# Kernel tuning notes

Measured on AMD Instinct MI355X. Metric: run time of the kernel, lower is better.

## Reference

```python
import jax, jax.numpy as jnp
import numpy as np

B, N, HC, HH, K, D = 64, 300, 64, 64, 3, 10

def setup_inputs() -> dict:
    key = jax.random.key(0)
    ks = jax.random.split(key, 8)
    inp = {
        "z": jax.random.normal(ks[0], (B, N, HC), dtype=jnp.float32),
        "W_in": jax.random.normal(ks[1], (HH, HC), dtype=jnp.float32) / np.sqrt(HC),
        "b_in": jax.random.normal(ks[2], (HH,), dtype=jnp.float32) * 0.01,
        "W_out": jax.random.normal(ks[3], (HC * HC, HH), dtype=jnp.float32) / np.sqrt(HH),
        "b_out": jax.random.normal(ks[4], (HC * HC,), dtype=jnp.float32) * 0.01,
        "node_emb": jax.random.normal(ks[5], (N, D), dtype=jnp.float32),
        "weights_pool": jax.random.normal(ks[6], (D, K, HH, HH), dtype=jnp.float32) / np.sqrt(D * HH),
        "bias_pool": jax.random.normal(ks[7], (D, HH), dtype=jnp.float32) * 0.01,
    }
    return inp

def _agc(z, node_emb, weights_pool, bias_pool):
    n = node_emb.shape[0]
    # data-adaptive adjacency: softmax over rows of relu(E E^T)
    supports = jax.nn.softmax(jax.nn.relu(node_emb @ node_emb.T), axis=1)  # [N,N]
    support_set = [jnp.eye(n, dtype=z.dtype), supports]
    for _ in range(2, K):  # Chebyshev recursion T_k = 2A T_{k-1} - T_{k-2}
        support_set.append(2.0 * supports @ support_set[-1] - support_set[-2])
    S = jnp.stack(support_set, axis=0)  # [K,N,N]
    weights = jnp.einsum('nd,dkio->nkio', node_emb, weights_pool)  # [N,K,HH,HH]
    bias = node_emb @ bias_pool  # [N,HH]
    x_g = jnp.einsum('knm,bmc->bnkc', S, z)  # [B,N,K,HH]
    return jnp.einsum('bnki,nkio->bno', x_g, weights) + bias

def reference(z, W_in, b_in, W_out, b_out, node_emb, weights_pool, bias_pool):
    h = jax.nn.relu(z @ W_in.T + b_in)                  # [B,N,HH]
    h = _agc(h, node_emb, weights_pool, bias_pool)      # [B,N,HH]
    out = (h @ W_out.T + b_out).reshape(B, N, HC, HC)   # [B,N,HC,HC]
    return jnp.tanh(out)
```

## Files before the change

kernel.cpp:

```cpp
#include <hip/hip_runtime.h>
#include <hip/hip_bf16.h>

#define BB 64
#define NN 300
#define HH 64
#define RTOT (BB*NN)
#define KIO  (3*HH*HH)
#define JOUT (HH*HH)

typedef __attribute__((ext_vector_type(8))) _Float16 f16x8;
typedef __attribute__((ext_vector_type(4))) float floatx4;

__device__ inline float tanh_fast(float x) {
    float e = __expf(2.f * x);
    return 1.f - 2.f * __builtin_amdgcn_rcpf(e + 1.f);
}

__global__ __launch_bounds__(256) void k_pre(const float* __restrict__ E,
                                             const float* __restrict__ z,
                                             const float* __restrict__ Win,
                                             const float* __restrict__ bin,
                                             const float* __restrict__ Wout,
                                             const float* __restrict__ pool,
                                             const float* __restrict__ bpool,
                                             float* __restrict__ A,
                                             float* __restrict__ h,
                                             float* __restrict__ Wn,
                                             float* __restrict__ bN,
                                             _Float16* __restrict__ Wh) {
    __shared__ float smem[8576];
    int bid = blockIdx.x, tid = threadIdx.x;

    if (bid < 300) {
        float* sE  = smem;
        float* row = smem + 16;
        float* red = smem + 320;
        int n = bid;
        if (tid < 10) sE[tid] = E[n*10 + tid];
        __syncthreads();
        float lmax = -1e30f;
        for (int m = tid; m < NN; m += 256) {
            float s = 0.f;
            #pragma unroll
            for (int d = 0; d < 10; ++d) s += sE[d] * E[m*10 + d];
            s = fmaxf(s, 0.f);
            row[m] = s;
            lmax = fmaxf(lmax, s);
        }
        red[tid] = lmax; __syncthreads();
        for (int off = 128; off > 0; off >>= 1) {
            if (tid < off) red[tid] = fmaxf(red[tid], red[tid+off]);
            __syncthreads();
        }
        float mx = red[0]; __syncthreads();
        float lsum = 0.f;
        for (int m = tid; m < NN; m += 256) {
            float e = __expf(row[m] - mx);
            row[m] = e;
            lsum += e;
        }
        red[tid] = lsum; __syncthreads();
        for (int off = 128; off > 0; off >>= 1) {
            if (tid < off) red[tid] += red[tid+off];
            __syncthreads();
        }
        float inv = 1.f / red[0];
        for (int m = tid; m < NN; m += 256) A[n*NN + m] = row[m] * inv;
    } else if (bid < 600) {
        float* Wt = smem;
        float* zl = smem + 4352;
        int tx = tid & 15, ty = tid >> 4;
        int r0 = (bid - 300) * 64;
        for (int e = tid; e < 4096; e += 256) {
            int o = e >> 6, c = e & 63;
            Wt[c*68 + o] = Win[e];
            zl[o*66 + c] = z[(size_t)(r0 + o)*64 + c];
        }
        __syncthreads();
        float4 bo = *(const float4*)&bin[tx*4];
        float acc[4][4];
        #pragma unroll
        for (int s = 0; s < 4; ++s) { acc[s][0]=bo.x; acc[s][1]=bo.y; acc[s][2]=bo.z; acc[s][3]=bo.w; }
        const float* zr = &zl[(ty*4)*66];
        for (int c = 0; c < 64; ++c) {
            float4 w = *(const float4*)&Wt[c*68 + tx*4];
            float z0 = zr[c], z1 = zr[66+c], z2 = zr[132+c], z3 = zr[198+c];
            acc[0][0] += z0*w.x; acc[0][1] += z0*w.y; acc[0][2] += z0*w.z; acc[0][3] += z0*w.w;
            acc[1][0] += z1*w.x; acc[1][1] += z1*w.y; acc[1][2] += z1*w.z; acc[1][3] += z1*w.w;
            acc[2][0] += z2*w.x; acc[2][1] += z2*w.y; acc[2][2] += z2*w.z; acc[2][3] += z2*w.w;
            acc[3][0] += z3*w.x; acc[3][1] += z3*w.y; acc[3][2] += z3*w.z; acc[3][3] += z3*w.w;
        }
        #pragma unroll
        for (int s = 0; s < 4; ++s) {
            float4 v = make_float4(fmaxf(acc[s][0],0.f), fmaxf(acc[s][1],0.f),
                                   fmaxf(acc[s][2],0.f), fmaxf(acc[s][3],0.f));
            *(float4*)&h[(size_t)(r0 + ty*4 + s)*64 + tx*4] = v;
        }
    } else if (bid < 675) {
        int idx = (bid - 600)*256 + tid;
        int n = idx >> 6, o = idx & 63;
        float s = 0.f;
        #pragma unroll
        for (int d = 0; d < 10; ++d) s += E[n*10 + d] * bpool[d*64 + o];
        bN[idx] = s;
    } else if (bid < 1699) {
        int idx = (bid - 675)*256 + tid;
        Wh[idx] = (_Float16)Wout[idx];
    } else {
        int idx = (bid - 1699)*256 + tid;
        int n = idx / KIO, kio = idx % KIO;
        float s = 0.f;
        #pragma unroll
        for (int d = 0; d < 10; ++d) s += E[n*10 + d] * pool[d*KIO + kio];
        Wn[idx] = s;
    }
}

__global__ __launch_bounds__(256) void k_spatialA(const float* __restrict__ A,
                                                  const float* __restrict__ h,
                                                  float* __restrict__ xg1) {
    int tid = threadIdx.x;
    int c = tid & 63;
    int w = __builtin_amdgcn_readfirstlane(tid >> 6);
    int b = blockIdx.y;
    int r0 = blockIdx.x * 20 + w * 5;
    const float* S = A + (size_t)r0 * NN;
    const float* hb = h + (size_t)b * NN * 64 + c;
    float a0 = 0.f, a1 = 0.f, a2 = 0.f, a3 = 0.f, a4 = 0.f;
    for (int m = 0; m < NN; m += 4) {
        float4 s0 = *(const float4*)(S + 0*NN + m);
        float4 s1 = *(const float4*)(S + 1*NN + m);
        float4 s2 = *(const float4*)(S + 2*NN + m);
        float4 s3 = *(const float4*)(S + 3*NN + m);
        float4 s4 = *(const float4*)(S + 4*NN + m);
        float h0 = hb[(m+0)*64];
        float h1 = hb[(m+1)*64];
        float h2 = hb[(m+2)*64];
        float h3 = hb[(m+3)*64];
        a0 = fmaf(s0.x,h0,a0); a0 = fmaf(s0.y,h1,a0); a0 = fmaf(s0.z,h2,a0); a0 = fmaf(s0.w,h3,a0);
        a1 = fmaf(s1.x,h0,a1); a1 = fmaf(s1.y,h1,a1); a1 = fmaf(s1.z,h2,a1); a1 = fmaf(s1.w,h3,a1);
        a2 = fmaf(s2.x,h0,a2); a2 = fmaf(s2.y,h1,a2); a2 = fmaf(s2.z,h2,a2); a2 = fmaf(s2.w,h3,a2);
        a3 = fmaf(s3.x,h0,a3); a3 = fmaf(s3.y,h1,a3); a3 = fmaf(s3.z,h2,a3); a3 = fmaf(s3.w,h3,a3);
        a4 = fmaf(s4.x,h0,a4); a4 = fmaf(s4.y,h1,a4); a4 = fmaf(s4.z,h2,a4); a4 = fmaf(s4.w,h3,a4);
    }
    float* dst = xg1 + ((size_t)b * NN + r0) * 64 + c;
    dst[0*64] = a0; dst[1*64] = a1; dst[2*64] = a2; dst[3*64] = a3; dst[4*64] = a4;
}

__global__ __launch_bounds__(256) void k_spatialB(const float* __restrict__ A,
                                                  const float* __restrict__ xg1,
                                                  const float* __restrict__ h,
                                                  float* __restrict__ xg2) {
    int tid = threadIdx.x;
    int c = tid & 63;
    int w = __builtin_amdgcn_readfirstlane(tid >> 6);
    int b = blockIdx.y;
    int r0 = blockIdx.x * 20 + w * 5;
    const float* S = A + (size_t)r0 * NN;
    const float* xb = xg1 + (size_t)b * NN * 64 + c;
    float a0 = 0.f, a1 = 0.f, a2 = 0.f, a3 = 0.f, a4 = 0.f;
    for (int m = 0; m < NN; m += 4) {
        float4 s0 = *(const float4*)(S + 0*NN + m);
        float4 s1 = *(const float4*)(S + 1*NN + m);
        float4 s2 = *(const float4*)(S + 2*NN + m);
        float4 s3 = *(const float4*)(S + 3*NN + m);
        float4 s4 = *(const float4*)(S + 4*NN + m);
        float x0 = xb[(m+0)*64];
        float x1 = xb[(m+1)*64];
        float x2 = xb[(m+2)*64];
        float x3 = xb[(m+3)*64];
        a0 = fmaf(s0.x,x0,a0); a0 = fmaf(s0.y,x1,a0); a0 = fmaf(s0.z,x2,a0); a0 = fmaf(s0.w,x3,a0);
        a1 = fmaf(s1.x,x0,a1); a1 = fmaf(s1.y,x1,a1); a1 = fmaf(s1.z,x2,a1); a1 = fmaf(s1.w,x3,a1);
        a2 = fmaf(s2.x,x0,a2); a2 = fmaf(s2.y,x1,a2); a2 = fmaf(s2.z,x2,a2); a2 = fmaf(s2.w,x3,a2);
        a3 = fmaf(s3.x,x0,a3); a3 = fmaf(s3.y,x1,a3); a3 = fmaf(s3.z,x2,a3); a3 = fmaf(s3.w,x3,a3);
        a4 = fmaf(s4.x,x0,a4); a4 = fmaf(s4.y,x1,a4); a4 = fmaf(s4.z,x2,a4); a4 = fmaf(s4.w,x3,a4);
    }
    const float* hb = h   + ((size_t)b * NN + r0) * 64 + c;
    float*       dst = xg2 + ((size_t)b * NN + r0) * 64 + c;
    dst[0*64] = 2.f*a0 - hb[0*64];
    dst[1*64] = 2.f*a1 - hb[1*64];
    dst[2*64] = 2.f*a2 - hb[2*64];
    dst[3*64] = 2.f*a3 - hb[3*64];
    dst[4*64] = 2.f*a4 - hb[4*64];
}

__global__ __launch_bounds__(256) void k_node_mm(const float* __restrict__ h,
                                                 const float* __restrict__ xg1,
                                                 const float* __restrict__ xg2,
                                                 const float* __restrict__ Wn,
                                                 const float* __restrict__ bN,
                                                 _Float16* __restrict__ h2h) {
    __shared__ float Wnl[192*64];
    __shared__ float xgl[8][192];
    int tid = threadIdx.x;
    int o = tid & 63, ty = tid >> 6;
    int n = blockIdx.x, b0 = blockIdx.y*8;
    for (int e = tid; e < 12288; e += 256) Wnl[e] = Wn[(size_t)n*KIO + e];
    for (int e = tid; e < 8*192; e += 256) {
        int bb = e / 192, ki = e % 192;
        int k = ki >> 6, i = ki & 63;
        const float* src = (k == 0) ? h : ((k == 1) ? xg1 : xg2);
        xgl[bb][ki] = src[((b0+bb)*NN + n)*64 + i];
    }
    __syncthreads();
    float bias = bN[n*64 + o];
    for (int bb = ty; bb < 8; bb += 4) {
        float acc = bias;
        for (int ki = 0; ki < 192; ++ki) acc += xgl[bb][ki] * Wnl[ki*64 + o];
        h2h[((b0+bb)*NN + n)*64 + o] = (_Float16)acc;
    }
}

__global__ __launch_bounds__(256) void k_out_proj_mfma(const _Float16* __restrict__ h2h,
                                                       const _Float16* __restrict__ Wh,
                                                       const float* __restrict__ bout,
                                                       float* __restrict__ out) {
    int tid  = threadIdx.x;
    int wave = tid >> 6, lane = tid & 63;
    int quad = lane >> 4, lr = lane & 15;
    int m0 = blockIdx.y*128 + (wave >> 1)*64;
    int n0 = blockIdx.x*128 + (wave & 1)*64;
    floatx4 acc[4][4] = {};
    const _Float16* Aptr = h2h + (size_t)(m0 + lr)*64 + quad*8;
    const _Float16* Bptr = Wh  + (size_t)(n0 + lr)*64 + quad*8;
    #pragma unroll
    for (int ks = 0; ks < 2; ++ks) {
        f16x8 a[4], b[4];
        #pragma unroll
        for (int f = 0; f < 4; ++f) {
            a[f] = *(const f16x8*)(Aptr + (size_t)f*16*64 + ks*32);
            b[f] = *(const f16x8*)(Bptr + (size_t)f*16*64 + ks*32);
        }
        #pragma unroll
        for (int mf = 0; mf < 4; ++mf)
            #pragma unroll
            for (int nf = 0; nf < 4; ++nf)
                acc[mf][nf] = __builtin_amdgcn_mfma_f32_16x16x32_f16(a[mf], b[nf], acc[mf][nf], 0, 0, 0);
    }
    #pragma unroll
    for (int nf = 0; nf < 4; ++nf) {
        int col = n0 + nf*16 + lr;
        float bj = bout[col];
        #pragma unroll
        for (int mf = 0; mf < 4; ++mf) {
            int row = m0 + mf*16 + quad*4;
            #pragma unroll
            for (int r = 0; r < 4; ++r) {
                float v = tanh_fast(acc[mf][nf][r] + bj);
                __builtin_nontemporal_store(v, &out[(size_t)(row + r)*JOUT + col]);
            }
        }
    }
}

extern "C" void kernel_launch(void* const* d_in, const int* in_sizes, int n_in,
                              void* d_out, int out_size, void* d_ws, size_t ws_size,
                              hipStream_t stream) {
    const float* z     = (const float*)d_in[0];
    const float* Win   = (const float*)d_in[1];
    const float* bin   = (const float*)d_in[2];
    const float* Wout  = (const float*)d_in[3];
    const float* bout  = (const float*)d_in[4];
    const float* E     = (const float*)d_in[5];
    const float* pool  = (const float*)d_in[6];
    const float* bpool = (const float*)d_in[7];
    float* out = (float*)d_out;

    float* ws  = (float*)d_ws;
    float* A   = ws;
    float* Wn  = A   + 90000;
    float* bN  = Wn  + 3686400;
    float* h   = bN  + 19200;
    float* xg1 = h   + 1228800;
    float* xg2 = xg1 + 1228800;
    _Float16* h2h   = (_Float16*)(xg2 + 1228800);
    _Float16* Wouth = h2h + 1228800;

    k_pre      <<<16099, 256, 0, stream>>>(E, z, Win, bin, Wout, pool, bpool,
                                           A, h, Wn, bN, Wouth);
    k_spatialA <<<dim3(15, BB), 256, 0, stream>>>(A, h, xg1);
    k_spatialB <<<dim3(15, BB), 256, 0, stream>>>(A, xg1, h, xg2);
    k_node_mm  <<<dim3(NN, 8), 256, 0, stream>>>(h, xg1, xg2, Wn, bN, h2h);
    k_out_proj_mfma<<<dim3(JOUT/128, RTOT/128), 256, 0, stream>>>(h2h, Wouth, bout, out);
}
```

Before: 454.6 us.

## Precompute Chebyshev T2 matrix and fuse spatial passes; retile node matmul

Computes the second Chebyshev support T2 = 2A·A − I once as an N×N matrix in a new kernel. The two dependent spatial passes then merge into one kernel that multiplies h by both A and T2 together, which removes the serialized second pass and the re-read of xg1. The per-node matmul is retiled so each block handles 32 batches with 8 outputs per thread, using vectorized loads, an XOR-swizzled shared layout and packed f16 stores. The cost is an extra small kernel launch, and T2 is formed in fp32 instead of applying A twice, which slightly changes rounding order.

```diff
diff --git a/kernel.cpp b/kernel.cpp
--- a/kernel.cpp
+++ b/kernel.cpp
@@ -116,72 +116,61 @@
     }
 }
 
-__global__ __launch_bounds__(256) void k_spatialA(const float* __restrict__ A,
-                                                  const float* __restrict__ h,
-                                                  float* __restrict__ xg1) {
+__global__ __launch_bounds__(256) void k_cheb(const float* __restrict__ A,
+                                              float* __restrict__ T2) {
+    __shared__ float Ar[NN];
+    int n = blockIdx.x, tid = threadIdx.x;
+    for (int m = tid; m < NN; m += 256) Ar[m] = A[n*NN + m];
+    __syncthreads();
+    for (int m = tid; m < NN; m += 256) {
+        float s = 0.f;
+        #pragma unroll 4
+        for (int l = 0; l < NN; ++l) s += Ar[l] * A[l*NN + m];
+        T2[n*NN + m] = 2.f*s - (n == m ? 1.f : 0.f);
+    }
+}
+
+__global__ __launch_bounds__(256) void k_spatial_both(const float* __restrict__ A,
+                                                      const float* __restrict__ T2,
+                                                      const float* __restrict__ h,
+                                                      float* __restrict__ xg1,
+                                                      float* __restrict__ xg2) {
     int tid = threadIdx.x;
     int c = tid & 63;
     int w = __builtin_amdgcn_readfirstlane(tid >> 6);
     int b = blockIdx.y;
     int r0 = blockIdx.x * 20 + w * 5;
-    const float* S = A + (size_t)r0 * NN;
+    const float* SA = A  + (size_t)r0 * NN;
+    const float* ST = T2 + (size_t)r0 * NN;
     const float* hb = h + (size_t)b * NN * 64 + c;
-    float a0 = 0.f, a1 = 0.f, a2 = 0.f, a3 = 0.f, a4 = 0.f;
+    float accA[5] = {0.f,0.f,0.f,0.f,0.f};
+    float accT[5] = {0.f,0.f,0.f,0.f,0.f};
     for (int m = 0; m < NN; m += 4) {
-        float4 s0 = *(const float4*)(S + 0*NN + m);
-        float4 s1 = *(const float4*)(S + 1*NN + m);
-        float4 s2 = *(const float4*)(S + 2*NN + m);
-        float4 s3 = *(const float4*)(S + 3*NN + m);
-        float4 s4 = *(const float4*)(S + 4*NN + m);
+        float4 sa[5], st[5];
+        #pragma unroll
+        for (int i = 0; i < 5; ++i) {
+            sa[i] = *(const float4*)(SA + i*NN + m);
+            st[i] = *(const float4*)(ST + i*NN + m);
+        }
         float h0 = hb[(m+0)*64];
         float h1 = hb[(m+1)*64];
         float h2 = hb[(m+2)*64];
         float h3 = hb[(m+3)*64];
-        a0 = fmaf(s0.x,h0,a0); a0 = fmaf(s0.y,h1,a0); a0 = fmaf(s0.z,h2,a0); a0 = fmaf(s0.w,h3,a0);
-        a1 = fmaf(s1.x,h0,a1); a1 = fmaf(s1.y,h1,a1); a1 = fmaf(s1.z,h2,a1); a1 = fmaf(s1.w,h3,a1);
-        a2 = fmaf(s2.x,h0,a2); a2 = fmaf(s2.y,h1,a2); a2 = fmaf(s2.z,h2,a2); a2 = fmaf(s2.w,h3,a2);
-        a3 = fmaf(s3.x,h0,a3); a3 = fmaf(s3.y,h1,a3); a3 = fmaf(s3.z,h2,a3); a3 = fmaf(s3.w,h3,a3);
-        a4 = fmaf(s4.x,h0,a4); a4 = fmaf(s4.y,h1,a4); a4 = fmaf(s4.z,h2,a4); a4 = fmaf(s4.w,h3,a4);
-    }
-    float* dst = xg1 + ((size_t)b * NN + r0) * 64 + c;
-    dst[0*64] = a0; dst[1*64] = a1; dst[2*64] = a2; dst[3*64] = a3; dst[4*64] = a4;
-}
-
-__global__ __launch_bounds__(256) void k_spatialB(const float* __restrict__ A,
-                                                  const float* __restrict__ xg1,
-                                                  const float* __restrict__ h,
-                                                  float* __restrict__ xg2) {
-    int tid = threadIdx.x;
-    int c = tid & 63;
-    int w = __builtin_amdgcn_readfirstlane(tid >> 6);
-    int b = blockIdx.y;
-    int r0 = blockIdx.x * 20 + w * 5;
-    const float* S = A + (size_t)r0 * NN;
-    const float* xb = xg1 + (size_t)b * NN * 64 + c;
-    float a0 = 0.f, a1 = 0.f, a2 = 0.f, a3 = 0.f, a4 = 0.f;
-    for (int m = 0; m < NN; m += 4) {
-        float4 s0 = *(const float4*)(S + 0*NN + m);
-        float4 s1 = *(const float4*)(S + 1*NN + m);
-        float4 s2 = *(const float4*)(S + 2*NN + m);
-        float4 s3 = *(const float4*)(S + 3*NN + m);
-        float4 s4 = *(const float4*)(S + 4*NN + m);
-        float x0 = xb[(m+0)*64];
-        float x1 = xb[(m+1)*64];
-        float x2 = xb[(m+2)*64];
-        float x3 = xb[(m+3)*64];
-        a0 = fmaf(s0.x,x0,a0); a0 = fmaf(s0.y,x1,a0); a0 = fmaf(s0.z,x2,a0); a0 = fmaf(s0.w,x3,a0);
-        a1 = fmaf(s1.x,x0,a1); a1 = fmaf(s1.y,x1,a1); a1 = fmaf(s1.z,x2,a1); a1 = fmaf(s1.w,x3,a1);
-        a2 = fmaf(s2.x,x0,a2); a2 = fmaf(s2.y,x1,a2); a2 = fmaf(s2.z,x2,a2); a2 = fmaf(s2.w,x3,a2);
-        a3 = fmaf(s3.x,x0,a3); a3 = fmaf(s3.y,x1,a3); a3 = fmaf(s3.z,x2,a3); a3 = fmaf(s3.w,x3,a3);
-        a4 = fmaf(s4.x,x0,a4); a4 = fmaf(s4.y,x1,a4); a4 = fmaf(s4.z,x2,a4); a4 = fmaf(s4.w,x3,a4);
-    }
-    const float* hb = h   + ((size_t)b * NN + r0) * 64 + c;
-    float*       dst = xg2 + ((size_t)b * NN + r0) * 64 + c;
-    dst[0*64] = 2.f*a0 - hb[0*64];
-    dst[1*64] = 2.f*a1 - hb[1*64];
-    dst[2*64] = 2.f*a2 - hb[2*64];
-    dst[3*64] = 2.f*a3 - hb[3*64];
-    dst[4*64] = 2.f*a4 - hb[4*64];
+        #pragma unroll
+        for (int i = 0; i < 5; ++i) {
+            accA[i] = fmaf(sa[i].x,h0,accA[i]); accA[i] = fmaf(sa[i].y,h1,accA[i]);
+            accA[i] = fmaf(sa[i].z,h2,accA[i]); accA[i] = fmaf(sa[i].w,h3,accA[i]);
+            accT[i] = fmaf(st[i].x,h0,accT[i]); accT[i] = fmaf(st[i].y,h1,accT[i]);
+            accT[i] = fmaf(st[i].z,h2,accT[i]); accT[i] = fmaf(st[i].w,h3,accT[i]);
+        }
+    }
+    float* d1 = xg1 + ((size_t)b * NN + r0) * 64 + c;
+    float* d2 = xg2 + ((size_t)b * NN + r0) * 64 + c;
+    #pragma unroll
+    for (int i = 0; i < 5; ++i) {
+        d1[i*64] = accA[i];
+        d2[i*64] = accT[i];
+    }
 }
 
 __global__ __launch_bounds__(256) void k_node_mm(const float* __restrict__ h,
@@ -190,25 +179,46 @@
                                                  const float* __restrict__ Wn,
                                                  const float* __restrict__ bN,
                                                  _Float16* __restrict__ h2h) {
-    __shared__ float Wnl[192*64];
-    __shared__ float xgl[8][192];
+    __shared__ float Wnl[12288];
+    __shared__ float xgl[6144];
     int tid = threadIdx.x;
-    int o = tid & 63, ty = tid >> 6;
-    int n = blockIdx.x, b0 = blockIdx.y*8;
-    for (int e = tid; e < 12288; e += 256) Wnl[e] = Wn[(size_t)n*KIO + e];
-    for (int e = tid; e < 8*192; e += 256) {
-        int bb = e / 192, ki = e % 192;
-        int k = ki >> 6, i = ki & 63;
+    int n = blockIdx.x, b_base = blockIdx.y * 32;
+
+    const float4* Wsrc = (const float4*)(Wn + (size_t)n*KIO);
+    for (int e4 = tid; e4 < 3072; e4 += 256) ((float4*)Wnl)[e4] = Wsrc[e4];
+
+    for (int e4 = tid; e4 < 1536; e4 += 256) {
+        int gi = e4 * 4;
+        int bl = gi / 192, kb = gi % 192;
+        int k = kb >> 6, i = kb & 63;
         const float* src = (k == 0) ? h : ((k == 1) ? xg1 : xg2);
-        xgl[bb][ki] = src[((b0+bb)*NN + n)*64 + i];
+        float4 v = *(const float4*)&src[((size_t)(b_base + bl)*NN + n)*64 + i];
+        xgl[(kb+0)*32 + (bl ^ ((kb+0)&31))] = v.x;
+        xgl[(kb+1)*32 + (bl ^ ((kb+1)&31))] = v.y;
+        xgl[(kb+2)*32 + (bl ^ ((kb+2)&31))] = v.z;
+        xgl[(kb+3)*32 + (bl ^ ((kb+3)&31))] = v.w;
     }
     __syncthreads();
-    float bias = bN[n*64 + o];
-    for (int bb = ty; bb < 8; bb += 4) {
-        float acc = bias;
-        for (int ki = 0; ki < 192; ++ki) acc += xgl[bb][ki] * Wnl[ki*64 + o];
-        h2h[((b0+bb)*NN + n)*64 + o] = (_Float16)acc;
-    }
+
+    int bl = tid & 31;
+    int o0 = (tid >> 5) * 8;
+    float acc[8];
+    #pragma unroll
+    for (int j = 0; j < 8; ++j) acc[j] = bN[n*64 + o0 + j];
+
+    for (int ki = 0; ki < 192; ++ki) {
+        float x = xgl[ki*32 + (bl ^ (ki & 31))];
+        float4 w0 = *(const float4*)&Wnl[ki*64 + o0];
+        float4 w1 = *(const float4*)&Wnl[ki*64 + o0 + 4];
+        acc[0] = fmaf(x, w0.x, acc[0]); acc[1] = fmaf(x, w0.y, acc[1]);
+        acc[2] = fmaf(x, w0.z, acc[2]); acc[3] = fmaf(x, w0.w, acc[3]);
+        acc[4] = fmaf(x, w1.x, acc[4]); acc[5] = fmaf(x, w1.y, acc[5]);
+        acc[6] = fmaf(x, w1.z, acc[6]); acc[7] = fmaf(x, w1.w, acc[7]);
+    }
+    f16x8 v;
+    #pragma unroll
+    for (int j = 0; j < 8; ++j) v[j] = (_Float16)acc[j];
+    *(f16x8*)&h2h[((size_t)(b_base + bl)*NN + n)*64 + o0] = v;
 }
 
 __global__ __launch_bounds__(256) void k_out_proj_mfma(const _Float16* __restrict__ h2h,
@@ -268,7 +278,8 @@
 
     float* ws  = (float*)d_ws;
     float* A   = ws;
-    float* Wn  = A   + 90000;
+    float* T2  = A   + 90000;
+    float* Wn  = T2  + 90000;
     float* bN  = Wn  + 3686400;
     float* h   = bN  + 19200;
     float* xg1 = h   + 1228800;
@@ -276,10 +287,10 @@
     _Float16* h2h   = (_Float16*)(xg2 + 1228800);
     _Float16* Wouth = h2h + 1228800;
 
-    k_pre      <<<16099, 256, 0, stream>>>(E, z, Win, bin, Wout, pool, bpool,
-                                           A, h, Wn, bN, Wouth);
-    k_spatialA <<<dim3(15, BB), 256, 0, stream>>>(A, h, xg1);
-    k_spatialB <<<dim3(15, BB), 256, 0, stream>>>(A, xg1, h, xg2);
-    k_node_mm  <<<dim3(NN, 8), 256, 0, stream>>>(h, xg1, xg2, Wn, bN, h2h);
+    k_pre         <<<16099, 256, 0, stream>>>(E, z, Win, bin, Wout, pool, bpool,
+                                              A, h, Wn, bN, Wouth);
+    k_cheb        <<<NN, 256, 0, stream>>>(A, T2);
+    k_spatial_both<<<dim3(15, BB), 256, 0, stream>>>(A, T2, h, xg1, xg2);
+    k_node_mm     <<<dim3(NN, 2), 256, 0, stream>>>(h, xg1, xg2, Wn, bN, h2h);
     k_out_proj_mfma<<<dim3(JOUT/128, RTOT/128), 256, 0, stream>>>(h2h, Wouth, bout, out);
 }
```

Measured after the change: 480.9 us. +5.8%, slower.
